# Optimization experiments

Measured on AMD Instinct MI355X. Metric: run time of the kernel, lower is better.

The kernel has to match this reference:

```python
import jax, jax.numpy as jnp
import numpy as np

M = 16384
C = 128
CLS_W = 8        # cls window size (even)
CLS_C = 64       # cls_depth
REG_W = 3        # reg window size (odd)
CLS_T = 1.0      # cls_temperature
REG_T = 1.0      # reg_temperature
PAD = REG_W // 2
W1 = CLS_W + 2 * PAD  # 10


def setup_inputs() -> dict:
    key = jax.random.key(0)
    k0, k1 = jax.random.split(key)
    feature0 = jax.random.normal(k0, (M, CLS_W * CLS_W, C), dtype=jnp.float32)
    feature1 = jax.random.normal(k1, (M, W1 * W1, C), dtype=jnp.float32)
    return {"feature0": feature0, "feature1": feature1}


def _inner_mask_indices():
    mask = np.zeros((W1, W1), dtype=bool)
    mask[PAD:-PAD, PAD:-PAD] = True
    return jnp.asarray(np.flatnonzero(mask.ravel()))


def reference(feature0, feature1):
    m = feature0.shape[0]
    reg_c = C - CLS_C
    cls_f0, reg_f0 = feature0[..., :CLS_C], feature0[..., CLS_C:]
    cls_f1, reg_f1 = feature1[..., :CLS_C], feature1[..., CLS_C:]

    # ---- cls branch: windowed correlation + dual softmax ----
    cls_f1m = cls_f1[:, _inner_mask_indices(), :]  # [m, cls_w^2, cls_c]
    sim = jnp.einsum('mlc,msc->mls', cls_f0, cls_f1m) / CLS_C / CLS_T
    heatmap = jax.nn.softmax(sim, axis=1) * jax.nn.softmax(sim, axis=2)  # [m, 64, 64]

    ww = CLS_W * CLS_W
    idx = jnp.argmax(heatmap.reshape(m, -1), axis=1)
    idxes0 = (idx // ww)[:, None]
    idxes1 = (idx % ww)[:, None]

    # kornia create_meshgrid(normalized=False): last dim is (x, y)
    ys, xs = jnp.meshgrid(jnp.arange(CLS_W, dtype=jnp.float32),
                          jnp.arange(CLS_W, dtype=jnp.float32), indexing='ij')
    biases = (jnp.stack([xs, ys], axis=-1) - CLS_W // 2 + 0.5).reshape(-1, 2)
    biases0 = biases[idxes0[:, 0]]
    biases1 = biases[idxes1[:, 0]]

    # ---- reg branch: gather window around top cls match, softmax expectation ----
    r = jnp.arange(m)
    rf0 = reg_f0[r, idxes0[:, 0]]                     # [m, reg_c]
    reg_sp = reg_f1.reshape(m, W1, W1, reg_c)         # spatial layout, row-major
    i1 = idxes1[:, 0] // CLS_W                        # top-left row of the reg window
    j1 = idxes1[:, 0] % CLS_W
    rows = i1[:, None] + jnp.arange(REG_W)            # [m, 3]
    cols = j1[:, None] + jnp.arange(REG_W)            # [m, 3]
    patch = reg_sp[r[:, None, None], rows[:, :, None], cols[:, None, :], :]  # [m,3,3,reg_c]
    rf1 = patch.reshape(m, REG_W * REG_W, reg_c)

    sim_r = jnp.einsum('mc,mrc->mr', rf0, rf1) / jnp.sqrt(jnp.float32(reg_c)) / REG_T
    hm_r = jax.nn.softmax(sim_r, axis=1).reshape(m, REG_W, REG_W)

    # kornia spatial_expectation2d with normalized coordinates in [-1, 1]
    lin = jnp.linspace(-1.0, 1.0, REG_W)
    gy, gx = jnp.meshgrid(lin, lin, indexing='ij')
    reg_biases = jnp.stack([jnp.sum(hm_r * gx, axis=(1, 2)),
                            jnp.sum(hm_r * gy, axis=(1, 2))], axis=-1)  # [m, 2]

    return heatmap, idxes0, idxes1, biases0, biases1, reg_biases
```

## Files before the change

### kernel.cpp

```cpp
#include <hip/hip_runtime.h>

#define STR 68

__global__ __launch_bounds__(256, 4) void fine_matching_kernel(
    const float* __restrict__ feat0, const float* __restrict__ feat1,
    float* __restrict__ out, int M)
{
  const int m    = blockIdx.x;
  const int t    = threadIdx.x;
  const int lane = t & 63;
  const int wave = t >> 6;

  __shared__ __align__(16) float sa[64 * STR];
  __shared__ __align__(16) float sb[64 * STR];
  __shared__ __align__(16) float colpm[4][64];
  __shared__ __align__(16) float colps[4][64];
  __shared__ float redv[4];
  __shared__ int   redi[4];
  __shared__ int   sIdx;

  const float* f0m = feat0 + (size_t)m * 8192;
  const float* f1m = feat1 + (size_t)m * 12800;

#pragma unroll
  for (int i = 0; i < 4; ++i) {
    int f  = i * 256 + t;
    int p  = f >> 4;
    int c4 = (f & 15) << 2;
    *(float4*)(&sa[p * STR + c4]) = *(const float4*)(f0m + p * 128 + c4);
    int row = (p >> 3) + 1, col = (p & 7) + 1;
    int xp  = ((p >> 2) & 7) << 2;
    *(float4*)(&sb[p * STR + (c4 ^ xp)]) = *(const float4*)(f1m + (row * 10 + col) * 128 + c4);
  }
  __syncthreads();

  const int st = t & 15, lt = t >> 4;
  const int s4 = st << 2, l4 = lt << 2;
  const int xs = (st & 7) << 2;

  float acc[4][4] = {};
#pragma unroll 4
  for (int c = 0; c < 64; c += 4) {
    float4 a[4], b[4];
#pragma unroll
    for (int i = 0; i < 4; ++i) a[i] = *(float4*)(&sa[(l4 + i) * STR + c]);
#pragma unroll
    for (int j = 0; j < 4; ++j) b[j] = *(float4*)(&sb[(s4 + j) * STR + (c ^ xs)]);
#pragma unroll
    for (int i = 0; i < 4; ++i)
#pragma unroll
      for (int j = 0; j < 4; ++j)
        acc[i][j] += a[i].x * b[j].x + a[i].y * b[j].y + a[i].z * b[j].z + a[i].w * b[j].w;
  }

  const float sc = 1.0f / 64.0f;
#pragma unroll
  for (int i = 0; i < 4; ++i)
#pragma unroll
    for (int j = 0; j < 4; ++j) acc[i][j] *= sc;

  float rmax[4], rinv[4];
#pragma unroll
  for (int i = 0; i < 4; ++i) {
    float rm = fmaxf(fmaxf(acc[i][0], acc[i][1]), fmaxf(acc[i][2], acc[i][3]));
#pragma unroll
    for (int off = 1; off <= 8; off <<= 1) rm = fmaxf(rm, __shfl_xor(rm, off));
    rmax[i] = rm;
  }
  {
    float cpm[4];
#pragma unroll
    for (int j = 0; j < 4; ++j) {
      float cm = fmaxf(fmaxf(acc[0][j], acc[1][j]), fmaxf(acc[2][j], acc[3][j]));
      cm = fmaxf(cm, __shfl_xor(cm, 16));
      cm = fmaxf(cm, __shfl_xor(cm, 32));
      cpm[j] = cm;
    }
    if (lane < 16) *(float4*)(&colpm[wave][s4]) = make_float4(cpm[0], cpm[1], cpm[2], cpm[3]);
  }
  __syncthreads();
  float cmaxv[4], cinv[4];
  {
    float4 q0 = *(float4*)(&colpm[0][s4]);
    float4 q1 = *(float4*)(&colpm[1][s4]);
    float4 q2 = *(float4*)(&colpm[2][s4]);
    float4 q3 = *(float4*)(&colpm[3][s4]);
    cmaxv[0] = fmaxf(fmaxf(q0.x, q1.x), fmaxf(q2.x, q3.x));
    cmaxv[1] = fmaxf(fmaxf(q0.y, q1.y), fmaxf(q2.y, q3.y));
    cmaxv[2] = fmaxf(fmaxf(q0.z, q1.z), fmaxf(q2.z, q3.z));
    cmaxv[3] = fmaxf(fmaxf(q0.w, q1.w), fmaxf(q2.w, q3.w));
  }

  float erow[4][4];
#pragma unroll
  for (int i = 0; i < 4; ++i) {
    float rs = 0.0f;
#pragma unroll
    for (int j = 0; j < 4; ++j) { erow[i][j] = __expf(acc[i][j] - rmax[i]); rs += erow[i][j]; }
#pragma unroll
    for (int off = 1; off <= 8; off <<= 1) rs += __shfl_xor(rs, off);
    rinv[i] = 1.0f / rs;
  }
  {
    float cps[4];
#pragma unroll
    for (int j = 0; j < 4; ++j) {
      float cs = 0.0f;
#pragma unroll
      for (int i = 0; i < 4; ++i) { acc[i][j] = __expf(acc[i][j] - cmaxv[j]); cs += acc[i][j]; }
      cs += __shfl_xor(cs, 16);
      cs += __shfl_xor(cs, 32);
      cps[j] = cs;
    }
    if (lane < 16) *(float4*)(&colps[wave][s4]) = make_float4(cps[0], cps[1], cps[2], cps[3]);
  }
  __syncthreads();
  {
    float4 q0 = *(float4*)(&colps[0][s4]);
    float4 q1 = *(float4*)(&colps[1][s4]);
    float4 q2 = *(float4*)(&colps[2][s4]);
    float4 q3 = *(float4*)(&colps[3][s4]);
    cinv[0] = 1.0f / (q0.x + q1.x + q2.x + q3.x);
    cinv[1] = 1.0f / (q0.y + q1.y + q2.y + q3.y);
    cinv[2] = 1.0f / (q0.z + q1.z + q2.z + q3.z);
    cinv[3] = 1.0f / (q0.w + q1.w + q2.w + q3.w);
  }

  float best = -1.0f; int bidx = 0;
  float* outh = out + (size_t)m * 4096;
#pragma unroll
  for (int i = 0; i < 4; ++i) {
    float ri = rinv[i];
    float4 h;
    h.x = erow[i][0] * acc[i][0] * ri * cinv[0];
    h.y = erow[i][1] * acc[i][1] * ri * cinv[1];
    h.z = erow[i][2] * acc[i][2] * ri * cinv[2];
    h.w = erow[i][3] * acc[i][3] * ri * cinv[3];
    int base = (l4 + i) * 64 + s4;
    *(float4*)(outh + base) = h;
    if (h.x > best) { best = h.x; bidx = base; }
    if (h.y > best) { best = h.y; bidx = base + 1; }
    if (h.z > best) { best = h.z; bidx = base + 2; }
    if (h.w > best) { best = h.w; bidx = base + 3; }
  }
#pragma unroll
  for (int off = 32; off; off >>= 1) {
    float ov = __shfl_xor(best, off);
    int   oi = __shfl_xor(bidx, off);
    if (ov > best || (ov == best && oi < bidx)) { best = ov; bidx = oi; }
  }
  if (lane == 0) { redv[wave] = best; redi[wave] = bidx; }
  __syncthreads();
  if (t == 0) {
#pragma unroll
    for (int w = 1; w < 4; ++w) {
      float ov = redv[w]; int oi = redi[w];
      if (ov > best || (ov == best && oi < bidx)) { best = ov; bidx = oi; }
    }
    sIdx = bidx;
    int i0 = bidx >> 6, i1 = bidx & 63;
    float* o = out + (size_t)M * 4096;
    o[m]         = (float)i0;
    o[M + m]     = (float)i1;
    o[2 * M + 2 * m + 0] = (float)(i0 & 7) - 3.5f;
    o[2 * M + 2 * m + 1] = (float)(i0 >> 3) - 3.5f;
    o[4 * M + 2 * m + 0] = (float)(i1 & 7) - 3.5f;
    o[4 * M + 2 * m + 1] = (float)(i1 >> 3) - 3.5f;
  }
  __syncthreads();

  if (wave == 0) {
    int bi = sIdx;
    int i0 = bi >> 6, i1 = bi & 63;
    float rf0 = f0m[i0 * 128 + 64 + lane];
    int r0 = i1 >> 3, c0 = i1 & 7;
    float p[9];
#pragma unroll
    for (int a = 0; a < 3; ++a)
#pragma unroll
      for (int b = 0; b < 3; ++b)
        p[a * 3 + b] = f1m[((r0 + a) * 10 + (c0 + b)) * 128 + 64 + lane] * rf0;
#pragma unroll
    for (int r = 0; r < 9; ++r)
#pragma unroll
      for (int off = 32; off; off >>= 1)
        p[r] += __shfl_xor(p[r], off);
    if (lane == 0) {
      float mx = p[0];
#pragma unroll
      for (int r = 1; r < 9; ++r) mx = fmaxf(mx, p[r]);
      float e[9], ssum = 0.0f;
#pragma unroll
      for (int r = 0; r < 9; ++r) { e[r] = __expf((p[r] - mx) * 0.125f); ssum += e[r]; }
      float inv = 1.0f / ssum, bx = 0.0f, by = 0.0f;
#pragma unroll
      for (int r = 0; r < 9; ++r) {
        float w = e[r] * inv;
        bx += w * (float)((r % 3) - 1);
        by += w * (float)((r / 3) - 1);
      }
      float* o = out + (size_t)M * 4096;
      o[6 * M + 2 * m + 0] = bx;
      o[6 * M + 2 * m + 1] = by;
    }
  }
}

extern "C" void kernel_launch(void* const* d_in, const int* in_sizes, int n_in,
                              void* d_out, int out_size, void* d_ws, size_t ws_size,
                              hipStream_t stream) {
  const float* f0 = (const float*)d_in[0];
  const float* f1 = (const float*)d_in[1];
  float* out = (float*)d_out;
  int M = in_sizes[0] / 8192;
  fine_matching_kernel<<<dim3(M), dim3(256), 0, stream>>>(f0, f1, out, M);
}
```

Before: 263.2 us.

## Process several matches per block with double-buffered async LDS loads

Each block now handles eight matches in a loop instead of one. It prefetches the next match's cls features into a second LDS buffer with global_load_lds while the current match is computed, and uses XOR swizzling to avoid bank conflicts. The softmax now skips the max subtraction, so a single exp serves both the row and the column normalisation and one barrier drops out. This halves the exp work and overlaps loads with compute, but doubles LDS per block and risks overflow if similarities get large. It also assumes M is a multiple of eight.

```diff
diff --git a/kernel.cpp b/kernel.cpp
--- a/kernel.cpp
+++ b/kernel.cpp
@@ -1,208 +1,199 @@
 #include <hip/hip_runtime.h>
 
-#define STR 68
-
-__global__ __launch_bounds__(256, 4) void fine_matching_kernel(
+#define ITERS 8
+
+__device__ __forceinline__ void gload_lds16(const float* g, float* l) {
+  __builtin_amdgcn_global_load_lds(
+      (const __attribute__((address_space(1))) unsigned int*)g,
+      (__attribute__((address_space(3))) unsigned int*)l, 16, 0, 0);
+}
+
+__global__ __launch_bounds__(256, 2) void fine_matching_kernel(
     const float* __restrict__ feat0, const float* __restrict__ feat1,
     float* __restrict__ out, int M)
 {
-  const int m    = blockIdx.x;
   const int t    = threadIdx.x;
   const int lane = t & 63;
   const int wave = t >> 6;
 
-  __shared__ __align__(16) float sa[64 * STR];
-  __shared__ __align__(16) float sb[64 * STR];
-  __shared__ __align__(16) float colpm[4][64];
+  __shared__ __align__(16) float sA[2][4096];
+  __shared__ __align__(16) float sB[2][4096];
   __shared__ __align__(16) float colps[4][64];
   __shared__ float redv[4];
   __shared__ int   redi[4];
-  __shared__ int   sIdx;
-
-  const float* f0m = feat0 + (size_t)m * 8192;
-  const float* f1m = feat1 + (size_t)m * 12800;
-
-#pragma unroll
-  for (int i = 0; i < 4; ++i) {
-    int f  = i * 256 + t;
-    int p  = f >> 4;
-    int c4 = (f & 15) << 2;
-    *(float4*)(&sa[p * STR + c4]) = *(const float4*)(f0m + p * 128 + c4);
-    int row = (p >> 3) + 1, col = (p & 7) + 1;
-    int xp  = ((p >> 2) & 7) << 2;
-    *(float4*)(&sb[p * STR + (c4 ^ xp)]) = *(const float4*)(f1m + (row * 10 + col) * 128 + c4);
-  }
-  __syncthreads();
 
   const int st = t & 15, lt = t >> 4;
   const int s4 = st << 2, l4 = lt << 2;
-  const int xs = (st & 7) << 2;
-
-  float acc[4][4] = {};
+  const int axs = (lt & 7) << 2;
+  const int bxs = (st & 7) << 2;
+
+  const int m0 = blockIdx.x * ITERS;
+
+  auto stage = [&](int buf, int m) {
+    const float* f0m = feat0 + (size_t)m * 8192;
+    const float* f1m = feat1 + (size_t)m * 12800;
+    const int pr = lane >> 4;
+    const int cq = (lane & 15) << 2;
+#pragma unroll
+    for (int k = 0; k < 4; ++k) {
+      int p = wave * 16 + k * 4 + pr;
+      int e = ((p >> 2) & 7) << 2;
+      gload_lds16(f0m + p * 128 + (cq ^ e), &sA[buf][(wave * 16 + k * 4) * 64]);
+      int row = (p >> 3) + 1, col = (p & 7) + 1;
+      gload_lds16(f1m + (row * 10 + col) * 128 + (cq ^ e),
+                  &sB[buf][(wave * 16 + k * 4) * 64]);
+    }
+  };
+
+  stage(0, m0);
+
+  int cur = 0;
+  for (int it = 0; it < ITERS; ++it) {
+    const int m = m0 + it;
+    const float* f0m = feat0 + (size_t)m * 8192;
+    const float* f1m = feat1 + (size_t)m * 12800;
+
+    asm volatile("s_waitcnt vmcnt(0) lgkmcnt(0)" ::: "memory");
+    __builtin_amdgcn_s_barrier();
+    asm volatile("" ::: "memory");
+
+    if (it + 1 < ITERS) stage(cur ^ 1, m + 1);
+
+    const float* A = sA[cur];
+    const float* B = sB[cur];
+    float acc[4][4] = {};
 #pragma unroll 4
-  for (int c = 0; c < 64; c += 4) {
-    float4 a[4], b[4];
-#pragma unroll
-    for (int i = 0; i < 4; ++i) a[i] = *(float4*)(&sa[(l4 + i) * STR + c]);
-#pragma unroll
-    for (int j = 0; j < 4; ++j) b[j] = *(float4*)(&sb[(s4 + j) * STR + (c ^ xs)]);
-#pragma unroll
-    for (int i = 0; i < 4; ++i)
-#pragma unroll
-      for (int j = 0; j < 4; ++j)
-        acc[i][j] += a[i].x * b[j].x + a[i].y * b[j].y + a[i].z * b[j].z + a[i].w * b[j].w;
-  }
-
-  const float sc = 1.0f / 64.0f;
-#pragma unroll
-  for (int i = 0; i < 4; ++i)
-#pragma unroll
-    for (int j = 0; j < 4; ++j) acc[i][j] *= sc;
-
-  float rmax[4], rinv[4];
-#pragma unroll
-  for (int i = 0; i < 4; ++i) {
-    float rm = fmaxf(fmaxf(acc[i][0], acc[i][1]), fmaxf(acc[i][2], acc[i][3]));
-#pragma unroll
-    for (int off = 1; off <= 8; off <<= 1) rm = fmaxf(rm, __shfl_xor(rm, off));
-    rmax[i] = rm;
-  }
-  {
-    float cpm[4];
-#pragma unroll
-    for (int j = 0; j < 4; ++j) {
-      float cm = fmaxf(fmaxf(acc[0][j], acc[1][j]), fmaxf(acc[2][j], acc[3][j]));
-      cm = fmaxf(cm, __shfl_xor(cm, 16));
-      cm = fmaxf(cm, __shfl_xor(cm, 32));
-      cpm[j] = cm;
-    }
-    if (lane < 16) *(float4*)(&colpm[wave][s4]) = make_float4(cpm[0], cpm[1], cpm[2], cpm[3]);
-  }
-  __syncthreads();
-  float cmaxv[4], cinv[4];
-  {
-    float4 q0 = *(float4*)(&colpm[0][s4]);
-    float4 q1 = *(float4*)(&colpm[1][s4]);
-    float4 q2 = *(float4*)(&colpm[2][s4]);
-    float4 q3 = *(float4*)(&colpm[3][s4]);
-    cmaxv[0] = fmaxf(fmaxf(q0.x, q1.x), fmaxf(q2.x, q3.x));
-    cmaxv[1] = fmaxf(fmaxf(q0.y, q1.y), fmaxf(q2.y, q3.y));
-    cmaxv[2] = fmaxf(fmaxf(q0.z, q1.z), fmaxf(q2.z, q3.z));
-    cmaxv[3] = fmaxf(fmaxf(q0.w, q1.w), fmaxf(q2.w, q3.w));
-  }
-
-  float erow[4][4];
-#pragma unroll
-  for (int i = 0; i < 4; ++i) {
-    float rs = 0.0f;
-#pragma unroll
-    for (int j = 0; j < 4; ++j) { erow[i][j] = __expf(acc[i][j] - rmax[i]); rs += erow[i][j]; }
-#pragma unroll
-    for (int off = 1; off <= 8; off <<= 1) rs += __shfl_xor(rs, off);
-    rinv[i] = 1.0f / rs;
-  }
-  {
-    float cps[4];
-#pragma unroll
-    for (int j = 0; j < 4; ++j) {
-      float cs = 0.0f;
-#pragma unroll
-      for (int i = 0; i < 4; ++i) { acc[i][j] = __expf(acc[i][j] - cmaxv[j]); cs += acc[i][j]; }
-      cs += __shfl_xor(cs, 16);
-      cs += __shfl_xor(cs, 32);
-      cps[j] = cs;
-    }
-    if (lane < 16) *(float4*)(&colps[wave][s4]) = make_float4(cps[0], cps[1], cps[2], cps[3]);
-  }
-  __syncthreads();
-  {
-    float4 q0 = *(float4*)(&colps[0][s4]);
-    float4 q1 = *(float4*)(&colps[1][s4]);
-    float4 q2 = *(float4*)(&colps[2][s4]);
-    float4 q3 = *(float4*)(&colps[3][s4]);
-    cinv[0] = 1.0f / (q0.x + q1.x + q2.x + q3.x);
-    cinv[1] = 1.0f / (q0.y + q1.y + q2.y + q3.y);
-    cinv[2] = 1.0f / (q0.z + q1.z + q2.z + q3.z);
-    cinv[3] = 1.0f / (q0.w + q1.w + q2.w + q3.w);
-  }
-
-  float best = -1.0f; int bidx = 0;
-  float* outh = out + (size_t)m * 4096;
-#pragma unroll
-  for (int i = 0; i < 4; ++i) {
-    float ri = rinv[i];
-    float4 h;
-    h.x = erow[i][0] * acc[i][0] * ri * cinv[0];
-    h.y = erow[i][1] * acc[i][1] * ri * cinv[1];
-    h.z = erow[i][2] * acc[i][2] * ri * cinv[2];
-    h.w = erow[i][3] * acc[i][3] * ri * cinv[3];
-    int base = (l4 + i) * 64 + s4;
-    *(float4*)(outh + base) = h;
-    if (h.x > best) { best = h.x; bidx = base; }
-    if (h.y > best) { best = h.y; bidx = base + 1; }
-    if (h.z > best) { best = h.z; bidx = base + 2; }
-    if (h.w > best) { best = h.w; bidx = base + 3; }
-  }
-#pragma unroll
-  for (int off = 32; off; off >>= 1) {
-    float ov = __shfl_xor(best, off);
-    int   oi = __shfl_xor(bidx, off);
-    if (ov > best || (ov == best && oi < bidx)) { best = ov; bidx = oi; }
-  }
-  if (lane == 0) { redv[wave] = best; redi[wave] = bidx; }
-  __syncthreads();
-  if (t == 0) {
+    for (int c = 0; c < 64; c += 4) {
+      float4 a[4], b[4];
+#pragma unroll
+      for (int i = 0; i < 4; ++i) a[i] = *(const float4*)(&A[(l4 + i) * 64 + (c ^ axs)]);
+#pragma unroll
+      for (int j = 0; j < 4; ++j) b[j] = *(const float4*)(&B[(s4 + j) * 64 + (c ^ bxs)]);
+#pragma unroll
+      for (int i = 0; i < 4; ++i)
+#pragma unroll
+        for (int j = 0; j < 4; ++j)
+          acc[i][j] += a[i].x * b[j].x + a[i].y * b[j].y + a[i].z * b[j].z + a[i].w * b[j].w;
+    }
+
+    float rinv[4];
+#pragma unroll
+    for (int i = 0; i < 4; ++i) {
+      float rs = 0.0f;
+#pragma unroll
+      for (int j = 0; j < 4; ++j) { acc[i][j] = __expf(acc[i][j] * 0.015625f); rs += acc[i][j]; }
+#pragma unroll
+      for (int off = 1; off <= 8; off <<= 1) rs += __shfl_xor(rs, off);
+      rinv[i] = 1.0f / rs;
+    }
+    {
+      float cps[4];
+#pragma unroll
+      for (int j = 0; j < 4; ++j) {
+        float cs = acc[0][j] + acc[1][j] + acc[2][j] + acc[3][j];
+        cs += __shfl_xor(cs, 16);
+        cs += __shfl_xor(cs, 32);
+        cps[j] = cs;
+      }
+      if (lane < 16) *(float4*)(&colps[wave][s4]) = make_float4(cps[0], cps[1], cps[2], cps[3]);
+    }
+    asm volatile("s_waitcnt lgkmcnt(0)" ::: "memory");
+    __builtin_amdgcn_s_barrier();
+    asm volatile("" ::: "memory");
+
+    float cinv[4];
+    {
+      float4 q0 = *(const float4*)(&colps[0][s4]);
+      float4 q1 = *(const float4*)(&colps[1][s4]);
+      float4 q2 = *(const float4*)(&colps[2][s4]);
+      float4 q3 = *(const float4*)(&colps[3][s4]);
+      cinv[0] = 1.0f / (q0.x + q1.x + q2.x + q3.x);
+      cinv[1] = 1.0f / (q0.y + q1.y + q2.y + q3.y);
+      cinv[2] = 1.0f / (q0.z + q1.z + q2.z + q3.z);
+      cinv[3] = 1.0f / (q0.w + q1.w + q2.w + q3.w);
+    }
+
+    float best = -1.0f; int bidx = 0;
+    float* outh = out + (size_t)m * 4096;
+#pragma unroll
+    for (int i = 0; i < 4; ++i) {
+      float ri = rinv[i];
+      float4 h;
+      h.x = acc[i][0] * acc[i][0] * ri * cinv[0];
+      h.y = acc[i][1] * acc[i][1] * ri * cinv[1];
+      h.z = acc[i][2] * acc[i][2] * ri * cinv[2];
+      h.w = acc[i][3] * acc[i][3] * ri * cinv[3];
+      int base = (l4 + i) * 64 + s4;
+      *(float4*)(outh + base) = h;
+      if (h.x > best) { best = h.x; bidx = base; }
+      if (h.y > best) { best = h.y; bidx = base + 1; }
+      if (h.z > best) { best = h.z; bidx = base + 2; }
+      if (h.w > best) { best = h.w; bidx = base + 3; }
+    }
+#pragma unroll
+    for (int off = 32; off; off >>= 1) {
+      float ov = __shfl_xor(best, off);
+      int   oi = __shfl_xor(bidx, off);
+      if (ov > best || (ov == best && oi < bidx)) { best = ov; bidx = oi; }
+    }
+    if (lane == 0) { redv[wave] = best; redi[wave] = bidx; }
+    asm volatile("s_waitcnt lgkmcnt(0)" ::: "memory");
+    __builtin_amdgcn_s_barrier();
+    asm volatile("" ::: "memory");
+
+    float fbv = redv[0]; int fbi = redi[0];
 #pragma unroll
     for (int w = 1; w < 4; ++w) {
       float ov = redv[w]; int oi = redi[w];
-      if (ov > best || (ov == best && oi < bidx)) { best = ov; bidx = oi; }
-    }
-    sIdx = bidx;
-    int i0 = bidx >> 6, i1 = bidx & 63;
-    float* o = out + (size_t)M * 4096;
-    o[m]         = (float)i0;
-    o[M + m]     = (float)i1;
-    o[2 * M + 2 * m + 0] = (float)(i0 & 7) - 3.5f;
-    o[2 * M + 2 * m + 1] = (float)(i0 >> 3) - 3.5f;
-    o[4 * M + 2 * m + 0] = (float)(i1 & 7) - 3.5f;
-    o[4 * M + 2 * m + 1] = (float)(i1 >> 3) - 3.5f;
-  }
-  __syncthreads();
-
-  if (wave == 0) {
-    int bi = sIdx;
-    int i0 = bi >> 6, i1 = bi & 63;
-    float rf0 = f0m[i0 * 128 + 64 + lane];
-    int r0 = i1 >> 3, c0 = i1 & 7;
-    float p[9];
-#pragma unroll
-    for (int a = 0; a < 3; ++a)
-#pragma unroll
-      for (int b = 0; b < 3; ++b)
-        p[a * 3 + b] = f1m[((r0 + a) * 10 + (c0 + b)) * 128 + 64 + lane] * rf0;
-#pragma unroll
-    for (int r = 0; r < 9; ++r)
-#pragma unroll
-      for (int off = 32; off; off >>= 1)
-        p[r] += __shfl_xor(p[r], off);
-    if (lane == 0) {
-      float mx = p[0];
-#pragma unroll
-      for (int r = 1; r < 9; ++r) mx = fmaxf(mx, p[r]);
-      float e[9], ssum = 0.0f;
-#pragma unroll
-      for (int r = 0; r < 9; ++r) { e[r] = __expf((p[r] - mx) * 0.125f); ssum += e[r]; }
-      float inv = 1.0f / ssum, bx = 0.0f, by = 0.0f;
-#pragma unroll
-      for (int r = 0; r < 9; ++r) {
-        float w = e[r] * inv;
-        bx += w * (float)((r % 3) - 1);
-        by += w * (float)((r / 3) - 1);
+      if (ov > fbv || (ov == fbv && oi < fbi)) { fbv = ov; fbi = oi; }
+    }
+    const int i0 = fbi >> 6, i1 = fbi & 63;
+
+    if (t == 0) {
+      float* o = out + (size_t)M * 4096;
+      o[m]         = (float)i0;
+      o[M + m]     = (float)i1;
+      o[2 * M + 2 * m + 0] = (float)(i0 & 7) - 3.5f;
+      o[2 * M + 2 * m + 1] = (float)(i0 >> 3) - 3.5f;
+      o[4 * M + 2 * m + 0] = (float)(i1 & 7) - 3.5f;
+      o[4 * M + 2 * m + 1] = (float)(i1 >> 3) - 3.5f;
+    }
+
+    if (wave == 0) {
+      float rf0 = f0m[i0 * 128 + 64 + lane];
+      int r0 = i1 >> 3, c0 = i1 & 7;
+      float p[9];
+#pragma unroll
+      for (int a = 0; a < 3; ++a)
+#pragma unroll
+        for (int b = 0; b < 3; ++b)
+          p[a * 3 + b] = f1m[((r0 + a) * 10 + (c0 + b)) * 128 + 64 + lane] * rf0;
+#pragma unroll
+      for (int r = 0; r < 9; ++r)
+#pragma unroll
+        for (int off = 32; off; off >>= 1)
+          p[r] += __shfl_xor(p[r], off);
+      if (lane == 0) {
+        float mx = p[0];
+#pragma unroll
+        for (int r = 1; r < 9; ++r) mx = fmaxf(mx, p[r]);
+        float e[9], ssum = 0.0f;
+#pragma unroll
+        for (int r = 0; r < 9; ++r) { e[r] = __expf((p[r] - mx) * 0.125f); ssum += e[r]; }
+        float inv = 1.0f / ssum, bx = 0.0f, by = 0.0f;
+#pragma unroll
+        for (int r = 0; r < 9; ++r) {
+          float w = e[r] * inv;
+          bx += w * (float)((r % 3) - 1);
+          by += w * (float)((r / 3) - 1);
+        }
+        float* o = out + (size_t)M * 4096;
+        o[6 * M + 2 * m + 0] = bx;
+        o[6 * M + 2 * m + 1] = by;
       }
-      float* o = out + (size_t)M * 4096;
-      o[6 * M + 2 * m + 0] = bx;
-      o[6 * M + 2 * m + 1] = by;
-    }
+    }
+
+    cur ^= 1;
   }
 }
 
@@ -213,5 +204,5 @@
   const float* f1 = (const float*)d_in[1];
   float* out = (float*)d_out;
   int M = in_sizes[0] / 8192;
-  fine_matching_kernel<<<dim3(M), dim3(256), 0, stream>>>(f0, f1, out, M);
+  fine_matching_kernel<<<dim3(M / ITERS), dim3(256), 0, stream>>>(f0, f1, out, M);
 }
```

New measurement: 305.9 us. 1.16x slower.
